# Kernel tuning notes

Hardware: AMD Instinct MI355X
Metric: run time of the kernel (lower is better)

The kernel has to match this reference:

```python
import jax, jax.numpy as jnp
import numpy as np
from jax import lax

STORAGE = 8
HIDDEN_HEAD = 32
N_BLOCKS = 16


def _conv(x, w, b, padding):
    # x: NCHW, w: OIHW
    y = lax.conv_general_dilated(
        x, w, window_strides=(1, 1), padding=padding,
        dimension_numbers=("NCHW", "OIHW", "NCHW"))
    return y + b[None, :, None, None]


def _min_pool3(x):
    # 3x3 sliding-window min, stride 1, same padding (pad value +inf so it
    return lax.reduce_window(x, float("inf"), lax.min,
                             (1, 1, 3, 3), (1, 1, 1, 1), "SAME")


def setup_inputs() -> dict:
    key = jax.random.key(0)
    ks = jax.random.split(key, 7)
    B, H, W = 8, 512, 512
    x = jax.random.normal(ks[0], (B, 1, H, W), dtype=jnp.float32)
    # initial 1x1 conv: 1 -> 8
    w0 = jax.random.normal(ks[1], (STORAGE, 1, 1, 1), dtype=jnp.float32) * 1.0
    b0 = jax.random.normal(ks[2], (STORAGE,), dtype=jnp.float32) * 0.1
    # head conv 3x3: 8 -> 32
    w1 = jax.random.normal(ks[3], (HIDDEN_HEAD, STORAGE, 3, 3), dtype=jnp.float32) * (1.0 / np.sqrt(STORAGE * 9))
    b1 = jax.random.normal(ks[4], (HIDDEN_HEAD,), dtype=jnp.float32) * 0.1
    # head conv 1x1: 32 -> 1
    w2 = jax.random.normal(ks[5], (1, HIDDEN_HEAD, 1, 1), dtype=jnp.float32) * (1.0 / np.sqrt(HIDDEN_HEAD))
    b2 = jax.random.normal(ks[6], (1,), dtype=jnp.float32) * 0.1
    return {"x": x, "w0": w0, "b0": b0, "w1": w1, "b1": b1, "w2": w2, "b2": b2}


def reference(x, w0, b0, w1, b1, w2, b2):
    h = _conv(x, w0, b0, "SAME")  # [B,8,H,W]
    for _ in range(N_BLOCKS):
        h = h + _min_pool3(h)
    h = _conv(h, w1, b1, "SAME")  # [B,32,H,W]
    h = jax.nn.relu(h)
    return _conv(h, w2, b2, "SAME")  # [B,1,H,W]
```

## Files before the change

kernel.cpp:

```cpp
#include <hip/hip_runtime.h>
#include <math.h>


#define N_PIX (512*512)
#define INF __builtin_inff()

typedef __attribute__((ext_vector_type(2))) float f2;

__global__ void prep_kernel(const float* __restrict__ w0, const float* __restrict__ b0,
                            const float* __restrict__ w1, const float* __restrict__ b1,
                            float* __restrict__ W)
{
    int tid = threadIdx.x;
    if (tid < 288) {
        int oc = tid / 9, k = tid - oc*9;
        float wp = 0.f, wq = 0.f;
        for (int ic = 0; ic < 8; ++ic) {
            float a = w0[ic];
            float w = w1[oc*72 + ic*9 + k];
            if (a > 0.f) wp += w * a;
            else         wq += w * (-a);
        }
        W[(oc*9 + k)*2 + 0] = wp;
        W[(oc*9 + k)*2 + 1] = wq;
        if (k == 0) {
            float beta[9];
            for (int kk = 0; kk < 9; ++kk) {
                float s = 0.f;
                for (int ic = 0; ic < 8; ++ic) s += b0[ic] * w1[oc*72 + ic*9 + kk];
                beta[kk] = 65536.0f * s;
            }
            for (int r = 0; r < 3; ++r) {
                W[576 + oc*4 + r] = beta[r*3] + beta[r*3+1] + beta[r*3+2]
                                  + ((r == 1) ? b1[oc] : 0.f);
                W[704 + oc*4 + r] = beta[r*3 + 0];
                W[832 + oc*4 + r] = beta[r*3 + 2];
            }
        }
    }
}

struct Row8 { float4 a, b; };

__device__ __forceinline__ Row8 row_update8(const Row8 up, const Row8 mid, const Row8 dn, int lane)
{
    float4 va, vb;
    va.x = fminf(fminf(up.a.x, mid.a.x), dn.a.x);
    va.y = fminf(fminf(up.a.y, mid.a.y), dn.a.y);
    va.z = fminf(fminf(up.a.z, mid.a.z), dn.a.z);
    va.w = fminf(fminf(up.a.w, mid.a.w), dn.a.w);
    vb.x = fminf(fminf(up.b.x, mid.b.x), dn.b.x);
    vb.y = fminf(fminf(up.b.y, mid.b.y), dn.b.y);
    vb.z = fminf(fminf(up.b.z, mid.b.z), dn.b.z);
    vb.w = fminf(fminf(up.b.w, mid.b.w), dn.b.w);
    float vmL = __shfl_up(vb.w, 1, 64);
    float vmR = __shfl_down(va.x, 1, 64);
    if (lane == 0)  vmL = INF;
    if (lane == 63) vmR = INF;
    float tm1 = fminf(vmL, va.x);
    float t0 = fminf(va.x, va.y), t1 = fminf(va.y, va.z);
    float t2 = fminf(va.z, va.w), t3 = fminf(va.w, vb.x);
    float t4 = fminf(vb.x, vb.y), t5 = fminf(vb.y, vb.z);
    float t6 = fminf(vb.z, vb.w), t7 = fminf(vb.w, vmR);
    Row8 o;
    o.a.x = mid.a.x + fminf(tm1, t0);
    o.a.y = mid.a.y + fminf(t0, t1);
    o.a.z = mid.a.z + fminf(t1, t2);
    o.a.w = mid.a.w + fminf(t2, t3);
    o.b.x = mid.b.x + fminf(t3, t4);
    o.b.y = mid.b.y + fminf(t4, t5);
    o.b.z = mid.b.z + fminf(t5, t6);
    o.b.w = mid.b.w + fminf(t6, t7);
    return o;
}

__global__ __launch_bounds__(512, 2) void erode16_kernel(
    const float* __restrict__ x, float* __restrict__ A)
{
    __shared__ float halo[2][8][2][8][64];
    const int tid   = threadIdx.x;
    const int lane  = tid & 63;
    const int w     = tid >> 6;
    const int ty    = blockIdx.x;
    const int plane = blockIdx.y;
    const int colg  = lane * 8;
    const int row0g = ty*32 - 16 + w*8;

    const float* sp = x + (plane & 7)*N_PIX;
    const float sgn = (plane >= 8) ? -1.f : 1.f;

    Row8 h[8];
    #pragma unroll
    for (int r = 0; r < 8; ++r) {
        int gy = row0g + r;
        if ((unsigned)gy < 512u) {
            const float* rp = sp + gy*512 + colg;
            float4 a = *(const float4*)rp;
            float4 b = *(const float4*)(rp + 4);
            h[r].a = make_float4(a.x*sgn, a.y*sgn, a.z*sgn, a.w*sgn);
            h[r].b = make_float4(b.x*sgn, b.y*sgn, b.z*sgn, b.w*sgn);
        } else {
            h[r].a = make_float4(INF, INF, INF, INF);
            h[r].b = h[r].a;
        }
    }

    const Row8 inf8 = { make_float4(INF,INF,INF,INF), make_float4(INF,INF,INF,INF) };
    for (int s = 0; s < 16; ++s) {
        int par = s & 1;
        {
            float* ht = &halo[par][w][0][0][lane];
            ht[0*64]=h[0].a.x; ht[1*64]=h[0].a.y; ht[2*64]=h[0].a.z; ht[3*64]=h[0].a.w;
            ht[4*64]=h[0].b.x; ht[5*64]=h[0].b.y; ht[6*64]=h[0].b.z; ht[7*64]=h[0].b.w;
            float* hb = &halo[par][w][1][0][lane];
            hb[0*64]=h[7].a.x; hb[1*64]=h[7].a.y; hb[2*64]=h[7].a.z; hb[3*64]=h[7].a.w;
            hb[4*64]=h[7].b.x; hb[5*64]=h[7].b.y; hb[6*64]=h[7].b.z; hb[7*64]=h[7].b.w;
        }
        Row8 n1 = row_update8(h[0], h[1], h[2], lane);
        Row8 n2 = row_update8(h[1], h[2], h[3], lane);
        Row8 n3 = row_update8(h[2], h[3], h[4], lane);
        Row8 n4 = row_update8(h[3], h[4], h[5], lane);
        Row8 n5 = row_update8(h[4], h[5], h[6], lane);
        Row8 n6 = row_update8(h[5], h[6], h[7], lane);
        __syncthreads();
        Row8 up = inf8, dn = inf8;
        if (w > 0) {
            const float* hu = &halo[par][w-1][1][0][lane];
            up.a.x=hu[0*64]; up.a.y=hu[1*64]; up.a.z=hu[2*64]; up.a.w=hu[3*64];
            up.b.x=hu[4*64]; up.b.y=hu[5*64]; up.b.z=hu[6*64]; up.b.w=hu[7*64];
        }
        if (w < 7) {
            const float* hd = &halo[par][w+1][0][0][lane];
            dn.a.x=hd[0*64]; dn.a.y=hd[1*64]; dn.a.z=hd[2*64]; dn.a.w=hd[3*64];
            dn.b.x=hd[4*64]; dn.b.y=hd[5*64]; dn.b.z=hd[6*64]; dn.b.w=hd[7*64];
        }
        Row8 n0 = row_update8(up,   h[0], h[1], lane);
        Row8 n7 = row_update8(h[6], h[7], dn,   lane);
        h[0]=n0; h[1]=n1; h[2]=n2; h[3]=n3; h[4]=n4; h[5]=n5; h[6]=n6; h[7]=n7;
    }

    if (w >= 2 && w <= 5) {
        float* dp = A + plane*N_PIX;
        #pragma unroll
        for (int r = 0; r < 8; ++r) {
            float* op = dp + (row0g + r)*512 + colg;
            *(float4*)op       = h[r].a;
            *(float4*)(op + 4) = h[r].b;
        }
    }
}

__global__ __launch_bounds__(256) void head_kernel(
    const float* __restrict__ A, const float* __restrict__ W,
    const float* __restrict__ w2, const float* __restrict__ b2,
    float* __restrict__ out)
{
    const int tid  = threadIdx.x;
    const int lane = tid & 63;
    const int w    = tid >> 6;
    const int img  = blockIdx.x >> 7;
    const int y    = (blockIdx.x & 127)*4 + w;
    const int x0   = lane*8;

    const float* P = A + img*N_PIX;
    const float* Q = A + (8 + img)*N_PIX;

    f2 pq[3][10];
    #pragma unroll
    for (int dy = 0; dy < 3; ++dy) {
        int gy = y + dy - 1;
        if ((unsigned)gy < 512u) {
            const float* rp = P + gy*512 + x0;
            const float* rq = Q + gy*512 + x0;
            float4 a = *(const float4*)rp;
            float4 b = *(const float4*)(rp + 4);
            float4 c = *(const float4*)rq;
            float4 d = *(const float4*)(rq + 4);
            pq[dy][1] = (f2){a.x, c.x}; pq[dy][2] = (f2){a.y, c.y};
            pq[dy][3] = (f2){a.z, c.z}; pq[dy][4] = (f2){a.w, c.w};
            pq[dy][5] = (f2){b.x, d.x}; pq[dy][6] = (f2){b.y, d.y};
            pq[dy][7] = (f2){b.z, d.z}; pq[dy][8] = (f2){b.w, d.w};
            float pl = __shfl_up(b.w, 1, 64),  ql = __shfl_up(d.w, 1, 64);
            float pr = __shfl_down(a.x, 1, 64), qr = __shfl_down(c.x, 1, 64);
            pq[dy][0] = (lane == 0)  ? (f2){0.f, 0.f} : (f2){pl, ql};
            pq[dy][9] = (lane == 63) ? (f2){0.f, 0.f} : (f2){pr, qr};
        } else {
            #pragma unroll
            for (int j = 0; j < 10; ++j) pq[dy][j] = (f2){0.f, 0.f};
        }
    }

    const float ry0 = (y >= 1)   ? 1.f : 0.f;
    const float ry2 = (y <= 510) ? 1.f : 0.f;
    const float mL  = (lane == 0)  ? -1.f : 0.f;
    const float mR  = (lane == 63) ? -1.f : 0.f;

    float o[8];
    #pragma unroll
    for (int j = 0; j < 8; ++j) o[j] = 0.f;

    const f2* Wv = (const f2*)W;
    #pragma unroll 2
    for (int oc = 0; oc < 32; ++oc) {
        f2 acc[8];
        {
            f2 wv0 = Wv[oc*9];
            #pragma unroll
            for (int j = 0; j < 8; ++j) acc[j] = wv0 * pq[0][j];
        }
        #pragma unroll
        for (int t = 1; t < 9; ++t) {
            const int ky = t / 3, kx = t - ky*3;
            f2 wv = Wv[oc*9 + t];
            #pragma unroll
            for (int j = 0; j < 8; ++j) acc[j] += wv * pq[ky][kx + j];
        }
        float base = W[576 + oc*4 + 1]
                   + ry0 * W[576 + oc*4 + 0]
                   + ry2 * W[576 + oc*4 + 2];
        float cl = W[704 + oc*4 + 1] + ry0 * W[704 + oc*4 + 0] + ry2 * W[704 + oc*4 + 2];
        float cr = W[832 + oc*4 + 1] + ry0 * W[832 + oc*4 + 0] + ry2 * W[832 + oc*4 + 2];
        float s[8];
        #pragma unroll
        for (int j = 0; j < 8; ++j) s[j] = acc[j].x + acc[j].y + base;
        s[0] = fmaf(cl, mL, s[0]);
        s[7] = fmaf(cr, mR, s[7]);
        float sc = w2[oc];
        #pragma unroll
        for (int j = 0; j < 8; ++j) o[j] += fmaxf(s[j], 0.f) * sc;
    }

    float bb = b2[0];
    float* op = out + img*N_PIX + y*512 + x0;
    *(float4*)(op)     = make_float4(o[0]+bb, o[1]+bb, o[2]+bb, o[3]+bb);
    *(float4*)(op + 4) = make_float4(o[4]+bb, o[5]+bb, o[6]+bb, o[7]+bb);
}

extern "C" void kernel_launch(void* const* d_in, const int* in_sizes, int n_in,
                              void* d_out, int out_size, void* d_ws, size_t ws_size,
                              hipStream_t stream) {
    const float* x  = (const float*)d_in[0];
    const float* w0 = (const float*)d_in[1];
    const float* b0 = (const float*)d_in[2];
    const float* w1 = (const float*)d_in[3];
    const float* b1 = (const float*)d_in[4];
    const float* w2 = (const float*)d_in[5];
    const float* b2 = (const float*)d_in[6];
    float* out = (float*)d_out;

    float* wsf = (float*)d_ws;
    float* A = wsf;
    float* W = wsf + 16*N_PIX;

    prep_kernel<<<1, 320, 0, stream>>>(w0, b0, w1, b1, W);

    dim3 eg(16, 16);
    erode16_kernel<<<eg, 512, 0, stream>>>(x, A);

    head_kernel<<<1024, 256, 0, stream>>>(A, W, w2, b2, out);
}
```

Baseline: 132.6 us.

## Split 16-step erosion into two 8-step passes with smaller tiles

The single fused 16-iteration erosion kernel becomes two launches of an 8-iteration kernel. The second launch reads an intermediate buffer written by the first. Blocks shrink from 512 to 256 threads with 16 output rows each, which doubles the grid and cheapens the per-step barrier. The row-update loop also now updates in place, which should lower register pressure. In exchange it adds a full round trip of the 16-plane intermediate through global memory, plus an extra kernel launch.

```diff
diff --git a/kernel.cpp b/kernel.cpp
--- a/kernel.cpp
+++ b/kernel.cpp
@@ -74,20 +74,22 @@
     return o;
 }
 
-__global__ __launch_bounds__(512, 2) void erode16_kernel(
-    const float* __restrict__ x, float* __restrict__ A)
-{
-    __shared__ float halo[2][8][2][8][64];
+__global__ __launch_bounds__(256) void erode8_kernel(
+    const float* __restrict__ src, float* __restrict__ dst, int first)
+{
+    __shared__ float halo[2][4][2][8][64];
     const int tid   = threadIdx.x;
     const int lane  = tid & 63;
     const int w     = tid >> 6;
     const int ty    = blockIdx.x;
     const int plane = blockIdx.y;
     const int colg  = lane * 8;
-    const int row0g = ty*32 - 16 + w*8;
-
-    const float* sp = x + (plane & 7)*N_PIX;
-    const float sgn = (plane >= 8) ? -1.f : 1.f;
+    const int row0g = ty*16 - 8 + w*8;
+
+    const float* sp;
+    float sgn = 1.f;
+    if (first) { sp = src + (plane & 7)*N_PIX; if (plane >= 8) sgn = -1.f; }
+    else       { sp = src + plane*N_PIX; }
 
     Row8 h[8];
     #pragma unroll
@@ -106,7 +108,7 @@
     }
 
     const Row8 inf8 = { make_float4(INF,INF,INF,INF), make_float4(INF,INF,INF,INF) };
-    for (int s = 0; s < 16; ++s) {
+    for (int s = 0; s < 8; ++s) {
         int par = s & 1;
         {
             float* ht = &halo[par][w][0][0][lane];
@@ -116,12 +118,14 @@
             hb[0*64]=h[7].a.x; hb[1*64]=h[7].a.y; hb[2*64]=h[7].a.z; hb[3*64]=h[7].a.w;
             hb[4*64]=h[7].b.x; hb[5*64]=h[7].b.y; hb[6*64]=h[7].b.z; hb[7*64]=h[7].b.w;
         }
-        Row8 n1 = row_update8(h[0], h[1], h[2], lane);
-        Row8 n2 = row_update8(h[1], h[2], h[3], lane);
-        Row8 n3 = row_update8(h[2], h[3], h[4], lane);
-        Row8 n4 = row_update8(h[3], h[4], h[5], lane);
-        Row8 n5 = row_update8(h[4], h[5], h[6], lane);
-        Row8 n6 = row_update8(h[5], h[6], h[7], lane);
+        Row8 o1 = h[1], o6 = h[6];
+        Row8 prev = h[0];
+        #pragma unroll
+        for (int r = 1; r <= 6; ++r) {
+            Row8 tmp = h[r];
+            h[r] = row_update8(prev, h[r], h[r+1], lane);
+            prev = tmp;
+        }
         __syncthreads();
         Row8 up = inf8, dn = inf8;
         if (w > 0) {
@@ -129,18 +133,17 @@
             up.a.x=hu[0*64]; up.a.y=hu[1*64]; up.a.z=hu[2*64]; up.a.w=hu[3*64];
             up.b.x=hu[4*64]; up.b.y=hu[5*64]; up.b.z=hu[6*64]; up.b.w=hu[7*64];
         }
-        if (w < 7) {
+        if (w < 3) {
             const float* hd = &halo[par][w+1][0][0][lane];
             dn.a.x=hd[0*64]; dn.a.y=hd[1*64]; dn.a.z=hd[2*64]; dn.a.w=hd[3*64];
             dn.b.x=hd[4*64]; dn.b.y=hd[5*64]; dn.b.z=hd[6*64]; dn.b.w=hd[7*64];
         }
-        Row8 n0 = row_update8(up,   h[0], h[1], lane);
-        Row8 n7 = row_update8(h[6], h[7], dn,   lane);
-        h[0]=n0; h[1]=n1; h[2]=n2; h[3]=n3; h[4]=n4; h[5]=n5; h[6]=n6; h[7]=n7;
-    }
-
-    if (w >= 2 && w <= 5) {
-        float* dp = A + plane*N_PIX;
+        h[0] = row_update8(up, h[0], o1, lane);
+        h[7] = row_update8(o6, h[7], dn, lane);
+    }
+
+    if (w == 1 || w == 2) {
+        float* dp = dst + plane*N_PIX;
         #pragma unroll
         for (int r = 0; r < 8; ++r) {
             float* op = dp + (row0g + r)*512 + colg;
@@ -250,12 +253,14 @@
 
     float* wsf = (float*)d_ws;
     float* A = wsf;
-    float* W = wsf + 16*N_PIX;
+    float* B = wsf + 16*N_PIX;
+    float* W = wsf + 32*N_PIX;
 
     prep_kernel<<<1, 320, 0, stream>>>(w0, b0, w1, b1, W);
 
-    dim3 eg(16, 16);
-    erode16_kernel<<<eg, 512, 0, stream>>>(x, A);
+    dim3 eg(32, 16);
+    erode8_kernel<<<eg, 256, 0, stream>>>(x, B, 1);
+    erode8_kernel<<<eg, 256, 0, stream>>>(B, A, 0);
 
     head_kernel<<<1024, 256, 0, stream>>>(A, W, w2, b2, out);
 }
```

Result: slower. 143.9 us (+8.5%).
